# Optimization experiments

Measured on AMD Instinct MI355X. Metric: run time of the kernel, lower is better.

## Reference

```python
import jax, jax.numpy as jnp
import numpy as np
from jax import lax

INPUT = 99
HIDDEN = 64
T = 65536


def setup_inputs() -> dict:
    key = jax.random.key(0)
    ks = jax.random.split(key, 8)
    x = jax.random.normal(ks[0], (1, T, INPUT), dtype=jnp.float32)
    # PyTorch LSTM params: weight_ih_l0 [4H, in], weight_hh_l0 [4H, H], biases [4H]
    s = 1.0 / np.sqrt(HIDDEN)
    W_ih = jax.random.uniform(ks[1], (4 * HIDDEN, INPUT), jnp.float32, -s, s)
    W_hh = jax.random.uniform(ks[2], (4 * HIDDEN, HIDDEN), jnp.float32, -s, s)
    b_ih = jax.random.uniform(ks[3], (4 * HIDDEN,), jnp.float32, -s, s)
    b_hh = jax.random.uniform(ks[4], (4 * HIDDEN,), jnp.float32, -s, s)
    # head: Linear(64->32, bias=False), Linear(32->3, bias=True)
    W1 = jax.random.normal(ks[5], (32, HIDDEN), dtype=jnp.float32) * 0.01
    W2 = jax.random.normal(ks[6], (3, 32), dtype=jnp.float32) * 0.01
    b2 = jnp.zeros((3,), dtype=jnp.float32)
    return {"x": x, "W_ih": W_ih, "W_hh": W_hh, "b_ih": b_ih, "b_hh": b_hh,
            "W1": W1, "W2": W2, "b2": b2}


def reference(x, W_ih, W_hh, b_ih, b_hh, W1, W2, b2):
    H = HIDDEN
    # Precompute input projections for all timesteps (one big GEMM).
    # x: [1, T, 99] -> xz: [T, 4H]; x[-1] == last (only) batch row.
    xz = jnp.einsum('td,gd->tg', x[-1], W_ih) + b_ih + b_hh

    def step(carry, z_t):
        h, c = carry
        z = z_t + W_hh @ h  # [4H]
        i, f, g, o = jnp.split(z, 4)  # PyTorch gate order: i, f, g, o
        i = jax.nn.sigmoid(i)
        f = jax.nn.sigmoid(f)
        g = jnp.tanh(g)
        o = jax.nn.sigmoid(o)
        c = f * c + i * g
        h = o * jnp.tanh(c)
        return (h, c), None

    h0 = jnp.zeros((H,), dtype=x.dtype)
    c0 = jnp.zeros((H,), dtype=x.dtype)
    (h_T, _), _ = lax.scan(step, (h0, c0), xz)

    # x[-1, -1] -> last timestep hidden of last batch row, then MLP head
    h = jax.nn.relu(h_T)
    h = jax.nn.relu(W1 @ h)
    out = W2 @ h + b2
    return out[None, :]  # [1, 3]
```

## Files before the change

kernel.cpp:

```cpp
#include <hip/hip_runtime.h>

#define T_STEPS 65536
#define NIN 99
#define HID 64
#define G4 256
#define TS 128
#define PF 8

__device__ __forceinline__ float frcp(float x) { return __builtin_amdgcn_rcpf(x); }
__device__ __forceinline__ float fexp(float x) { return __expf(x); }
__device__ __forceinline__ float sigmoid_f(float x) { return frcp(1.0f + fexp(-x)); }
__device__ __forceinline__ float tanh_f(float x) {
    float ax = fabsf(x);
    float e  = fexp(2.0f * ax);
    float r  = 1.0f - 2.0f * frcp(e + 1.0f);
    return copysignf(r, x);
}
__device__ __forceinline__ float bcast(float v, int lane) {
    return __int_as_float(__builtin_amdgcn_readlane(__float_as_int(v), lane));
}

#define BAR_LGKM() asm volatile("s_waitcnt lgkmcnt(0)\n\ts_barrier" ::: "memory")

__global__ __launch_bounds__(256, 1) void xz_kernel(
    const float* __restrict__ x, const float* __restrict__ W_ih,
    const float* __restrict__ b_ih, const float* __restrict__ b_hh,
    float* __restrict__ xz2) {
    __shared__ __align__(16) float xs[TS * 100];
    const int g  = threadIdx.x;
    const int t0 = blockIdx.x * TS;
    const int unit = g & 63, d = g >> 6;

    for (int i = g; i < TS * NIN; i += 256) {
        int tl = i / NIN;
        int j  = i - tl * NIN;
        xs[tl * 100 + j] = x[(size_t)t0 * NIN + i];
    }

    float w[NIN];
#pragma unroll
    for (int j = 0; j < NIN; ++j) w[j] = W_ih[g * NIN + j];
    const float bias = b_ih[g] + b_hh[g];
    __syncthreads();

    for (int tl = 0; tl < TS; ++tl) {
        const float* xr = &xs[tl * 100];
        float a0 = bias, a1 = 0.f, a2 = 0.f, a3 = 0.f;
#pragma unroll
        for (int j4 = 0; j4 < 24; ++j4) {
            float4 xv = *(const float4*)(xr + 4 * j4);
            a0 = fmaf(w[4 * j4 + 0], xv.x, a0);
            a1 = fmaf(w[4 * j4 + 1], xv.y, a1);
            a2 = fmaf(w[4 * j4 + 2], xv.z, a2);
            a3 = fmaf(w[4 * j4 + 3], xv.w, a3);
        }
        a0 = fmaf(w[96], xr[96], a0);
        a1 = fmaf(w[97], xr[97], a1);
        a2 = fmaf(w[98], xr[98], a2);
        xz2[(size_t)(t0 + tl) * G4 + unit * 4 + d] = (a0 + a1) + (a2 + a3);
    }
}

__global__ __launch_bounds__(256, 1) __attribute__((amdgpu_waves_per_eu(1)))
void lstm_kernel(
    const float* __restrict__ xz2, const float* __restrict__ W_hh,
    const float* __restrict__ W1, const float* __restrict__ W2,
    const float* __restrict__ b2, float* __restrict__ out) {
    __shared__ __align__(16) float4 pbuf[2][4][HID];
    __shared__ float hfin[HID];
    __shared__ float hbuf[32];
    const int tid = threadIdx.x;
    const int l   = tid & 63;
    const int wv  = tid >> 6;
    const int sb  = __builtin_amdgcn_readfirstlane(16 * wv);

    const float* Wb = W_hh + l * HID + sb;
    float4 wi0 = *(const float4*)(Wb +     0), wi1 = *(const float4*)(Wb +     4),
           wi2 = *(const float4*)(Wb +     8), wi3 = *(const float4*)(Wb +    12);
    float4 wf0 = *(const float4*)(Wb +  4096), wf1 = *(const float4*)(Wb +  4100),
           wf2 = *(const float4*)(Wb +  4104), wf3 = *(const float4*)(Wb +  4108);
    float4 wg0 = *(const float4*)(Wb +  8192), wg1 = *(const float4*)(Wb +  8196),
           wg2 = *(const float4*)(Wb +  8200), wg3 = *(const float4*)(Wb +  8204);
    float4 wo0 = *(const float4*)(Wb + 12288), wo1 = *(const float4*)(Wb + 12292),
           wo2 = *(const float4*)(Wb + 12296), wo3 = *(const float4*)(Wb + 12300);

#define PIN4(v) asm volatile("" : "+v"(v.x), "+v"(v.y), "+v"(v.z), "+v"(v.w))
    PIN4(wi0); PIN4(wi1); PIN4(wi2); PIN4(wi3);
    PIN4(wf0); PIN4(wf1); PIN4(wf2); PIN4(wf3);
    PIN4(wg0); PIN4(wg1); PIN4(wg2); PIN4(wg3);
    PIN4(wo0); PIN4(wo1); PIN4(wo2); PIN4(wo3);
#undef PIN4

    float h = 0.0f, c = 0.0f;

    const float* zi = xz2 + 4 * l;
    float4 zcur[PF], znxt[PF];
    if (wv == 0) {
#pragma unroll
        for (int p = 0; p < PF; ++p) zcur[p] = *(const float4*)(zi + (size_t)p * G4);
    }

#define STEP_J4(J4, WI, WF, WG, WO)                                             \
    {   float hx0 = bcast(h, sb + 4 * J4 + 0);                                  \
        float hx1 = bcast(h, sb + 4 * J4 + 1);                                  \
        float hx2 = bcast(h, sb + 4 * J4 + 2);                                  \
        float hx3 = bcast(h, sb + 4 * J4 + 3);                                  \
        ai = fmaf(WI.x, hx0, ai); ai = fmaf(WI.y, hx1, ai);                     \
        ai = fmaf(WI.z, hx2, ai); ai = fmaf(WI.w, hx3, ai);                     \
        af = fmaf(WF.x, hx0, af); af = fmaf(WF.y, hx1, af);                     \
        af = fmaf(WF.z, hx2, af); af = fmaf(WF.w, hx3, af);                     \
        ag = fmaf(WG.x, hx0, ag); ag = fmaf(WG.y, hx1, ag);                     \
        ag = fmaf(WG.z, hx2, ag); ag = fmaf(WG.w, hx3, ag);                     \
        ao = fmaf(WO.x, hx0, ao); ao = fmaf(WO.y, hx1, ao);                     \
        ao = fmaf(WO.z, hx2, ao); ao = fmaf(WO.w, hx3, ao); }

    for (int tb = 0; tb < T_STEPS; tb += PF) {
        if (wv == 0 && tb + PF < T_STEPS) {
#pragma unroll
            for (int p = 0; p < PF; ++p)
                znxt[p] = *(const float4*)(zi + (size_t)(tb + PF + p) * G4);
        }
#pragma unroll
        for (int u = 0; u < PF; ++u) {
            const int par = u & 1;
            float ai, af, ag, ao;
            if (wv == 0) { ai = zcur[u].x; af = zcur[u].y; ag = zcur[u].z; ao = zcur[u].w; }
            else         { ai = 0.f; af = 0.f; ag = 0.f; ao = 0.f; }
            STEP_J4(0, wi0, wf0, wg0, wo0)
            STEP_J4(1, wi1, wf1, wg1, wo1)
            STEP_J4(2, wi2, wf2, wg2, wo2)
            STEP_J4(3, wi3, wf3, wg3, wo3)
            pbuf[par][wv][l] = make_float4(ai, af, ag, ao);
            BAR_LGKM();

            float4 r0 = pbuf[par][(wv + 1) & 3][l];
            float4 r1 = pbuf[par][(wv + 2) & 3][l];
            float4 r2 = pbuf[par][(wv + 3) & 3][l];
            float si = (ai + r0.x) + (r1.x + r2.x);
            float sf = (af + r0.y) + (r1.y + r2.y);
            float sg = (ag + r0.z) + (r1.z + r2.z);
            float so = (ao + r0.w) + (r1.w + r2.w);
            float ig = sigmoid_f(si);
            float fg = sigmoid_f(sf);
            float gg = tanh_f(sg);
            float og = sigmoid_f(so);
            c = fmaf(fg, c, ig * gg);
            h = og * tanh_f(c);
        }
        if (wv == 0) {
#pragma unroll
            for (int p = 0; p < PF; ++p) zcur[p] = znxt[p];
        }
    }
#undef STEP_J4

    if (tid < HID) hfin[tid] = h;
    __syncthreads();
    if (tid < 32) {
        float s = 0.0f;
#pragma unroll
        for (int j = 0; j < HID; ++j) s += W1[tid * HID + j] * fmaxf(hfin[j], 0.0f);
        hbuf[tid] = fmaxf(s, 0.0f);
    }
    __syncthreads();
    if (tid < 3) {
        float s = b2[tid];
#pragma unroll
        for (int j = 0; j < 32; ++j) s += W2[tid * 32 + j] * hbuf[j];
        out[tid] = s;
    }
}

extern "C" void kernel_launch(void* const* d_in, const int* in_sizes, int n_in,
                              void* d_out, int out_size, void* d_ws, size_t ws_size,
                              hipStream_t stream) {
    const float* x   = (const float*)d_in[0];
    const float* Wih = (const float*)d_in[1];
    const float* Whh = (const float*)d_in[2];
    const float* bih = (const float*)d_in[3];
    const float* bhh = (const float*)d_in[4];
    const float* W1  = (const float*)d_in[5];
    const float* W2  = (const float*)d_in[6];
    const float* b2  = (const float*)d_in[7];
    float* out = (float*)d_out;
    float* xz2 = (float*)d_ws;

    xz_kernel<<<T_STEPS / TS, 256, 0, stream>>>(x, Wih, bih, bhh, xz2);
    lstm_kernel<<<1, 256, 0, stream>>>(xz2, Whh, W1, W2, b2, out);
}
```

Measured before the change: 22.91 ms.

## Use packed fp16 dot2 for recurrent matvec and spread xz prefetch across waves

Converts W_hh weights and the broadcast hidden state to packed fp16 pairs and uses v_dot2 instructions, halving the readlane broadcasts and FMAs on the serial recurrent path. The per-step input projection loads are distributed across all four waves instead of only wave 0, and exp is replaced with an exp2 builtin. This shortens the per-timestep critical path but introduces fp16 rounding of weights and hidden state (round-toward-zero), which over 65536 recurrent steps risks accuracy drift.

```diff
diff --git a/kernel.cpp b/kernel.cpp
--- a/kernel.cpp
+++ b/kernel.cpp
@@ -7,17 +7,34 @@
 #define TS 128
 #define PF 8
 
+typedef _Float16 half2v __attribute__((ext_vector_type(2)));
+
 __device__ __forceinline__ float frcp(float x) { return __builtin_amdgcn_rcpf(x); }
-__device__ __forceinline__ float fexp(float x) { return __expf(x); }
-__device__ __forceinline__ float sigmoid_f(float x) { return frcp(1.0f + fexp(-x)); }
+__device__ __forceinline__ float fexp2(float x) { return __builtin_amdgcn_exp2f(x); }
+
+#define LOG2E 1.4426950408889634f
+
+__device__ __forceinline__ float sigmoid_f(float x) { return frcp(1.0f + fexp2(x * -LOG2E)); }
 __device__ __forceinline__ float tanh_f(float x) {
     float ax = fabsf(x);
-    float e  = fexp(2.0f * ax);
+    float e  = fexp2(ax * (2.0f * LOG2E));
     float r  = 1.0f - 2.0f * frcp(e + 1.0f);
     return copysignf(r, x);
 }
-__device__ __forceinline__ float bcast(float v, int lane) {
-    return __int_as_float(__builtin_amdgcn_readlane(__float_as_int(v), lane));
+
+__device__ __forceinline__ half2v pk16(float a, float b) {
+#if __has_builtin(__builtin_amdgcn_cvt_pkrtz)
+    return __builtin_bit_cast(half2v, __builtin_amdgcn_cvt_pkrtz(a, b));
+#else
+    half2v r; r.x = (_Float16)a; r.y = (_Float16)b; return r;
+#endif
+}
+__device__ __forceinline__ float fdot2f(half2v a, half2v b, float c) {
+#if __has_builtin(__builtin_amdgcn_fdot2)
+    return __builtin_amdgcn_fdot2(a, b, c, false);
+#else
+    return fmaf((float)a.x, (float)b.x, fmaf((float)a.y, (float)b.y, c));
+#endif
 }
 
 #define BAR_LGKM() asm volatile("s_waitcnt lgkmcnt(0)\n\ts_barrier" ::: "memory")
@@ -75,61 +92,54 @@
     const int sb  = __builtin_amdgcn_readfirstlane(16 * wv);
 
     const float* Wb = W_hh + l * HID + sb;
-    float4 wi0 = *(const float4*)(Wb +     0), wi1 = *(const float4*)(Wb +     4),
-           wi2 = *(const float4*)(Wb +     8), wi3 = *(const float4*)(Wb +    12);
-    float4 wf0 = *(const float4*)(Wb +  4096), wf1 = *(const float4*)(Wb +  4100),
-           wf2 = *(const float4*)(Wb +  4104), wf3 = *(const float4*)(Wb +  4108);
-    float4 wg0 = *(const float4*)(Wb +  8192), wg1 = *(const float4*)(Wb +  8196),
-           wg2 = *(const float4*)(Wb +  8200), wg3 = *(const float4*)(Wb +  8204);
-    float4 wo0 = *(const float4*)(Wb + 12288), wo1 = *(const float4*)(Wb + 12292),
-           wo2 = *(const float4*)(Wb + 12296), wo3 = *(const float4*)(Wb + 12300);
-
-#define PIN4(v) asm volatile("" : "+v"(v.x), "+v"(v.y), "+v"(v.z), "+v"(v.w))
-    PIN4(wi0); PIN4(wi1); PIN4(wi2); PIN4(wi3);
-    PIN4(wf0); PIN4(wf1); PIN4(wf2); PIN4(wf3);
-    PIN4(wg0); PIN4(wg1); PIN4(wg2); PIN4(wg3);
-    PIN4(wo0); PIN4(wo1); PIN4(wo2); PIN4(wo3);
-#undef PIN4
+    int wiP[8], wfP[8], wgP[8], woP[8];
+#pragma unroll
+    for (int j = 0; j < 8; ++j) {
+        wiP[j] = __builtin_bit_cast(int, pk16(Wb[2 * j + 0],     Wb[2 * j + 1]));
+        wfP[j] = __builtin_bit_cast(int, pk16(Wb[2 * j + 4096],  Wb[2 * j + 4097]));
+        wgP[j] = __builtin_bit_cast(int, pk16(Wb[2 * j + 8192],  Wb[2 * j + 8193]));
+        woP[j] = __builtin_bit_cast(int, pk16(Wb[2 * j + 12288], Wb[2 * j + 12289]));
+        asm volatile("" : "+v"(wiP[j]), "+v"(wfP[j]), "+v"(wgP[j]), "+v"(woP[j]));
+    }
 
     float h = 0.0f, c = 0.0f;
 
     const float* zi = xz2 + 4 * l;
-    float4 zcur[PF], znxt[PF];
-    if (wv == 0) {
-#pragma unroll
-        for (int p = 0; p < PF; ++p) zcur[p] = *(const float4*)(zi + (size_t)p * G4);
-    }
-
-#define STEP_J4(J4, WI, WF, WG, WO)                                             \
-    {   float hx0 = bcast(h, sb + 4 * J4 + 0);                                  \
-        float hx1 = bcast(h, sb + 4 * J4 + 1);                                  \
-        float hx2 = bcast(h, sb + 4 * J4 + 2);                                  \
-        float hx3 = bcast(h, sb + 4 * J4 + 3);                                  \
-        ai = fmaf(WI.x, hx0, ai); ai = fmaf(WI.y, hx1, ai);                     \
-        ai = fmaf(WI.z, hx2, ai); ai = fmaf(WI.w, hx3, ai);                     \
-        af = fmaf(WF.x, hx0, af); af = fmaf(WF.y, hx1, af);                     \
-        af = fmaf(WF.z, hx2, af); af = fmaf(WF.w, hx3, af);                     \
-        ag = fmaf(WG.x, hx0, ag); ag = fmaf(WG.y, hx1, ag);                     \
-        ag = fmaf(WG.z, hx2, ag); ag = fmaf(WG.w, hx3, ag);                     \
-        ao = fmaf(WO.x, hx0, ao); ao = fmaf(WO.y, hx1, ao);                     \
-        ao = fmaf(WO.z, hx2, ao); ao = fmaf(WO.w, hx3, ao); }
+    float4 zc0 = *(const float4*)(zi + (size_t)(wv)     * G4);
+    float4 zc1 = *(const float4*)(zi + (size_t)(wv + 4) * G4);
+    float4 zn0 = make_float4(0.f, 0.f, 0.f, 0.f);
+    float4 zn1 = make_float4(0.f, 0.f, 0.f, 0.f);
 
     for (int tb = 0; tb < T_STEPS; tb += PF) {
-        if (wv == 0 && tb + PF < T_STEPS) {
-#pragma unroll
-            for (int p = 0; p < PF; ++p)
-                znxt[p] = *(const float4*)(zi + (size_t)(tb + PF + p) * G4);
+        if (tb + PF < T_STEPS) {
+            zn0 = *(const float4*)(zi + (size_t)(tb + PF + wv)     * G4);
+            zn1 = *(const float4*)(zi + (size_t)(tb + PF + wv + 4) * G4);
         }
 #pragma unroll
         for (int u = 0; u < PF; ++u) {
             const int par = u & 1;
             float ai, af, ag, ao;
-            if (wv == 0) { ai = zcur[u].x; af = zcur[u].y; ag = zcur[u].z; ao = zcur[u].w; }
-            else         { ai = 0.f; af = 0.f; ag = 0.f; ao = 0.f; }
-            STEP_J4(0, wi0, wf0, wg0, wo0)
-            STEP_J4(1, wi1, wf1, wg1, wo1)
-            STEP_J4(2, wi2, wf2, wg2, wo2)
-            STEP_J4(3, wi3, wf3, wg3, wo3)
+            if (wv == (u & 3)) {
+                float4 z = (u < 4) ? zc0 : zc1;
+                ai = z.x; af = z.y; ag = z.z; ao = z.w;
+            } else { ai = 0.f; af = 0.f; ag = 0.f; ao = 0.f; }
+
+#if __has_builtin(__builtin_amdgcn_mov_dpp)
+            float hn = __int_as_float(__builtin_amdgcn_mov_dpp(
+                __float_as_int(h), 0xB1 , 0xF, 0xF, true));
+#else
+            float hn = __shfl_xor(h, 1, 64);
+#endif
+            const int hpi = __builtin_bit_cast(int, pk16(h, hn));
+#pragma unroll
+            for (int j = 0; j < 8; ++j) {
+                half2v hpj = __builtin_bit_cast(half2v,
+                    __builtin_amdgcn_readlane(hpi, sb + 2 * j));
+                ai = fdot2f(__builtin_bit_cast(half2v, wiP[j]), hpj, ai);
+                af = fdot2f(__builtin_bit_cast(half2v, wfP[j]), hpj, af);
+                ag = fdot2f(__builtin_bit_cast(half2v, wgP[j]), hpj, ag);
+                ao = fdot2f(__builtin_bit_cast(half2v, woP[j]), hpj, ao);
+            }
             pbuf[par][wv][l] = make_float4(ai, af, ag, ao);
             BAR_LGKM();
 
@@ -147,12 +157,8 @@
             c = fmaf(fg, c, ig * gg);
             h = og * tanh_f(c);
         }
-        if (wv == 0) {
-#pragma unroll
-            for (int p = 0; p < PF; ++p) zcur[p] = znxt[p];
-        }
+        zc0 = zn0; zc1 = zn1;
     }
-#undef STEP_J4
 
     if (tid < HID) hfin[tid] = h;
     __syncthreads();
```

Measured after the change: 23.37 ms. +2.0%, slower.
